# Kernel tuning notes

Hardware: AMD Instinct MI355X
Metric: run time of the kernel (lower is better)

The kernel has to match this reference:

```python
import jax, jax.numpy as jnp
import numpy as np
import math

BS, SEQ, DIM, H, LK = 4, 4096, 768, 12, 256
HD = DIM // H  # 64
WIN = SEQ // LK  # 16, AdaptiveAvgPool1d reduces to uniform windows since SEQ % LK == 0


def setup_inputs() -> dict:
    key = jax.random.key(0)
    ks = jax.random.split(key, 12)
    s = 1.0 / math.sqrt(DIM)
    return {
        "query": jax.random.normal(ks[0], (BS, SEQ, DIM), jnp.float32),
        "key": jax.random.normal(ks[1], (BS, SEQ, DIM), jnp.float32),
        "value": jax.random.normal(ks[2], (BS, SEQ, DIM), jnp.float32),
        "mask": jax.random.normal(ks[3], (BS, SEQ), jnp.float32),  # mask<0 -> padded
        "Wq": jax.random.normal(ks[4], (DIM, DIM), jnp.float32) * s,
        "bq": jnp.zeros((DIM,), jnp.float32),
        "Wk": jax.random.normal(ks[5], (DIM, DIM), jnp.float32) * s,
        "bk": jnp.zeros((DIM,), jnp.float32),
        "Wv": jax.random.normal(ks[6], (DIM, DIM), jnp.float32) * s,
        "bv": jnp.zeros((DIM,), jnp.float32),
        "Wo": jax.random.normal(ks[7], (DIM, DIM), jnp.float32) * s,
        "bo": jnp.zeros((DIM,), jnp.float32),
    }


def reference(query, key, value, mask, Wq, bq, Wk, bk, Wv, bv, Wo, bo):
    bs, q_len, _ = query.shape
    # projections (nn.Linear: x @ W.T + b)
    Q = query @ Wq.T + bq
    K = key @ Wk.T + bk
    V = value @ Wv.T + bv
    # mask-fill padded K/V rows with 0 (mask dim==2 path: bool_mask = mask < 0)
    keep = (mask >= 0)[:, :, None]  # [bs, seq, 1]
    K = jnp.where(keep, K, 0.0)
    V = jnp.where(keep, V, 0.0)
    # adaptive avg pool over sequence -> linformer_k=256 (uniform windows of 16)
    Kc = K.reshape(bs, LK, WIN, DIM).mean(axis=2)  # [bs, 256, dim]
    Vc = V.reshape(bs, LK, WIN, DIM).mean(axis=2)
    # split heads
    Qh = Q.reshape(bs, q_len, H, HD) / math.sqrt(HD)  # scale fused
    Kh = Kc.reshape(bs, LK, H, HD)
    Vh = Vc.reshape(bs, LK, H, HD)
    # low-rank attention: [bs, h, q_len, 256]
    scores = jnp.einsum("bqhd,bkhd->bhqk", Qh, Kh)
    weights = jax.nn.softmax(scores, axis=-1)
    context = jnp.einsum("bhqk,bkhd->bqhd", weights, Vh).reshape(bs, q_len, DIM)
    return context @ Wo.T + bo
```

## Files before the change

kernel.cpp:

```cpp
#include <hip/hip_runtime.h>

#define BS_   4
#define SEQ_  4096
#define DIM_  768
#define NH_   12
#define HD_   64
#define LK_   256

typedef __attribute__((ext_vector_type(8))) short          bf8;
typedef __attribute__((ext_vector_type(8))) unsigned short us8;
typedef __attribute__((ext_vector_type(4))) unsigned short us4;
typedef __attribute__((ext_vector_type(4))) float          f32x4;
typedef __attribute__((ext_vector_type(4))) unsigned int   u32x4;

typedef unsigned int u32g __attribute__((address_space(1)));
typedef unsigned int u32l __attribute__((address_space(3)));

#define LOG2E 1.44269504088896340736f

__device__ __forceinline__ unsigned short f2bf(float f) {
  unsigned u = __builtin_bit_cast(unsigned, f);
  u += 0x7fffu + ((u >> 16) & 1u);
  return (unsigned short)(u >> 16);
}

__device__ __forceinline__ us8 cvt8(const float* __restrict__ p) {
  const float4 a = *(const float4*)p;
  const float4 b = *(const float4*)(p + 4);
  us8 r;
  r[0] = f2bf(a.x); r[1] = f2bf(a.y); r[2] = f2bf(a.z); r[3] = f2bf(a.w);
  r[4] = f2bf(b.x); r[5] = f2bf(b.y); r[6] = f2bf(b.z); r[7] = f2bf(b.w);
  return r;
}

__device__ __forceinline__ f32x4 max4(f32x4 a, f32x4 b) {
  f32x4 r;
  r[0] = fmaxf(a[0], b[0]); r[1] = fmaxf(a[1], b[1]);
  r[2] = fmaxf(a[2], b[2]); r[3] = fmaxf(a[3], b[3]);
  return r;
}

__device__ __forceinline__ float fexp2(float x) {
  float r; asm("v_exp_f32 %0, %1" : "=v"(r) : "v"(x)); return r;
}
__device__ __forceinline__ unsigned cvtpk(float lo, float hi) {
  unsigned r; asm("v_cvt_pk_bf16_f32 %0, %1, %2" : "=v"(r) : "v"(lo), "v"(hi));
  return r;
}

__global__ __launch_bounds__(384) void prep_kernel(
    const float* __restrict__ key, const float* __restrict__ value,
    const float* __restrict__ mask, const float* __restrict__ query,
    const float* __restrict__ Wq, const float* __restrict__ Wk,
    const float* __restrict__ Wv, const float* __restrict__ Wo,
    unsigned short* __restrict__ pk, unsigned short* __restrict__ pv,
    float* __restrict__ frac,
    unsigned short* __restrict__ Qbf, unsigned short* __restrict__ Wbf)
{
  const int bid = blockIdx.x;
  const int tid = threadIdx.x;
  if (bid < 1024) {
    const int b = bid >> 8;
    const int l = bid & 255;
    __shared__ float keep[16];
    if (tid < 16) keep[tid] = (mask[b * SEQ_ + l * 16 + tid] >= 0.f) ? 1.f : 0.f;
    __syncthreads();
    const int isV = tid >= 192;
    const int c = isV ? tid - 192 : tid;
    const float* src = isV ? value : key;
    const float* base = src + (size_t)(b * SEQ_ + l * 16) * DIM_ + c * 4;
    float4 acc = make_float4(0.f, 0.f, 0.f, 0.f);
    #pragma unroll
    for (int w = 0; w < 16; ++w) {
      const float4 v = *(const float4*)(base + (size_t)w * DIM_);
      const float kw = keep[w];
      acc.x = fmaf(kw, v.x, acc.x); acc.y = fmaf(kw, v.y, acc.y);
      acc.z = fmaf(kw, v.z, acc.z); acc.w = fmaf(kw, v.w, acc.w);
    }
    const float s = 1.f / 16.f;
    unsigned short* dst = isV ? pv : pk;
    us4 o4;
    o4[0] = f2bf(acc.x * s); o4[1] = f2bf(acc.y * s);
    o4[2] = f2bf(acc.z * s); o4[3] = f2bf(acc.w * s);
    *(us4*)(dst + (size_t)(b * LK_ + l) * DIM_ + c * 4) = o4;
    if (tid == 0) {
      float cnt = 0.f;
      for (int w = 0; w < 16; ++w) cnt += keep[w];
      frac[b * LK_ + l] = cnt * s;
    }
    return;
  }
  const int QN8 = (BS_ * SEQ_ * DIM_) / 8;
  const int WN8 = (DIM_ * DIM_) / 8;
  const int i0 = (bid - 1024) * 768 + tid;
  #pragma unroll
  for (int u = 0; u < 2; ++u) {
    const int i = i0 + u * 384;
    if (i < QN8) { *(us8*)(Qbf + (size_t)i * 8) = cvt8(query + (size_t)i * 8); continue; }
    int j = i - QN8;
    const float* src; unsigned short* dst;
    if      (j <     WN8) { src = Wq; dst = Wbf;                   }
    else if (j < 2 * WN8) { src = Wk; dst = Wbf + DIM_*DIM_;     j -=     WN8; }
    else if (j < 3 * WN8) { src = Wv; dst = Wbf + 2*DIM_*DIM_;   j -= 2 * WN8; }
    else if (j < 4 * WN8) { src = Wo; dst = Wbf + 3*DIM_*DIM_;   j -= 3 * WN8; }
    else continue;
    *(us8*)(dst + (size_t)j * 8) = cvt8(src + (size_t)j * 8);
  }
}

template<int MODE, int SWZ>
__global__ __launch_bounds__(256) void gemm_bt(
    const void* __restrict__ Aptr_, const void* __restrict__ Bptr_,
    const float* __restrict__ bias, const float* __restrict__ bias2,
    const float* __restrict__ frac,
    void* __restrict__ Cout, float scale)
{
  constexpr int K  = DIM_;
  constexpr int BK = 64;
  constexpr int NT = K / BK;
  __shared__ __align__(16) unsigned short lA[2][128 * BK];
  __shared__ __align__(16) unsigned short lB[2][128 * BK];
  const int tid  = threadIdx.x;
  const int lane = tid & 63;
  const int wave = tid >> 6;

  int bx, by;
  if (SWZ) {
    const int r = (blockIdx.x & 7) * 96 + (blockIdx.x >> 3);
    bx = r / 6; by = r % 6;
  } else {
    bx = blockIdx.x; by = blockIdx.y;
  }
  const int brow = bx * 128;
  const int bcol = by * 128;

  const unsigned short* A  = (const unsigned short*)Aptr_;
  const unsigned short* Bw = (const unsigned short*)Bptr_;
  const float* bb = bias;
  int isV = 0;
  if (MODE == 34) {
    isV = blockIdx.z;
    A  += (size_t)isV * (BS_ * LK_ * DIM_);
    Bw += (size_t)isV * (DIM_ * DIM_);
    if (isV) bb = bias2;
  }

  const int wr = (wave >> 1) * 64;
  const int wc = (wave & 1) * 64;
  const int fr = lane & 15;
  const int hi = lane >> 4;
  const int rx = fr & 7;

  f32x4 acc[4][4];
  #pragma unroll
  for (int i = 0; i < 4; ++i)
    #pragma unroll
    for (int j = 0; j < 4; ++j) acc[i][j] = (f32x4){0.f, 0.f, 0.f, 0.f};

  const int srow = tid >> 3;
  const int schk = ((tid & 7) ^ (srow & 7)) * 8;

  auto STAGE = [&](int t, int b) {
    const int k0 = t * BK;
    #pragma unroll
    for (int s = 0; s < 4; ++s) {
      __builtin_amdgcn_global_load_lds(
          (const u32g*)(A + (size_t)(brow + srow + s * 32) * K + k0 + schk),
          (u32l*)&lA[b][s * 2048 + tid * 8], 16, 0, 0);
      __builtin_amdgcn_global_load_lds(
          (const u32g*)(Bw + (size_t)(bcol + srow + s * 32) * K + k0 + schk),
          (u32l*)&lB[b][s * 2048 + tid * 8], 16, 0, 0);
    }
  };

  auto COMPUTE = [&](int b) {
    #pragma unroll
    for (int ks = 0; ks < 2; ++ks) {
      bf8 af[4], bfv[4];
      const int c = ks * 4 + hi;
      const int pc = (c ^ rx) * 8;
      #pragma unroll
      for (int mi = 0; mi < 4; ++mi)
        af[mi] = *(const bf8*)&lA[b][(wr + mi * 16 + fr) * BK + pc];
      #pragma unroll
      for (int ni = 0; ni < 4; ++ni)
        bfv[ni] = *(const bf8*)&lB[b][(wc + ni * 16 + fr) * BK + pc];
      #pragma unroll
      for (int mi = 0; mi < 4; ++mi)
        #pragma unroll
        for (int ni = 0; ni < 4; ++ni)
          acc[mi][ni] = __builtin_amdgcn_mfma_f32_16x16x32_bf16(af[mi], bfv[ni], acc[mi][ni], 0, 0, 0);
    }
  };

  STAGE(0, 0);
  STAGE(1, 1);
  asm volatile("s_waitcnt vmcnt(8)" ::: "memory");
  __builtin_amdgcn_s_barrier();

  #pragma unroll 2
  for (int t = 0; t < NT; ++t) {
    COMPUTE(t & 1);
    if (t + 1 < NT) {
      __builtin_amdgcn_s_barrier();
      if (t + 2 < NT) {
        STAGE(t + 2, t & 1);
        asm volatile("s_waitcnt vmcnt(8)" ::: "memory");
      } else {
        asm volatile("s_waitcnt vmcnt(0)" ::: "memory");
      }
      __builtin_amdgcn_s_barrier();
    }
  }

  const int er = (lane >> 4) * 4;
  #pragma unroll
  for (int mi = 0; mi < 4; ++mi) {
    #pragma unroll
    for (int ni = 0; ni < 4; ++ni) {
      #pragma unroll
      for (int j = 0; j < 4; ++j) {
        const int r = brow + wr + mi * 16 + er + j;
        const int c = bcol + wc + ni * 16 + fr;
        float v = acc[mi][ni][j];
        if (MODE == 0) {
          v = (v + bias[c]) * scale;
          ((unsigned short*)Cout)[(size_t)r * DIM_ + c] = f2bf(v);
        } else if (MODE == 2) {
          ((float*)Cout)[(size_t)r * DIM_ + c] = v + bias[c];
        } else {
          v += frac[r] * bb[c];
          const int bb_ = r >> 8, key = r & 255;
          const int hh = c >> 6, dd = c & 63;
          const int bh = bb_ * NH_ + hh;
          size_t idx;
          if (isV) {
            idx = (size_t)bh * 16384 +
                ((key >> 5) * 4 + (dd >> 4)) * 512 + ((key >> 3) & 3) * 128 +
                (dd & 15) * 8 + (key & 7) + 786432;
          } else {
            const int tt = key >> 5, g = (key >> 3) & 3, sub = (key >> 2) & 1, jj = key & 3;
            const int frk = g * 4 + jj;
            idx = (size_t)bh * 16384 +
                (((tt * 2 + sub) * 2) + (dd >> 5)) * 512 + ((dd >> 3) & 3) * 128 +
                frk * 8 + (dd & 7);
          }
          ((unsigned short*)Cout)[idx] = f2bf(v);
        }
      }
    }
  }
}

__global__ __launch_bounds__(512, 4) void attn_fused(
    const unsigned short* __restrict__ Qh,
    const unsigned short* __restrict__ Kf,
    const unsigned short* __restrict__ Vf,
    unsigned short* __restrict__ ctx)
{
  __shared__ __align__(16) unsigned short Ks[16384];
  const int tid  = threadIdx.x;
  const int lane = tid & 63;
  const int wave = tid >> 6;
  const int bh = blockIdx.y;
  const int b = bh / NH_, h = bh % NH_;
  const int fr = lane & 15;
  const int hi = lane >> 4;
  const int qrow = blockIdx.x * 128 + wave * 16;

  {
    const unsigned short* kg = Kf + (size_t)bh * 16384 + tid * 8;
    #pragma unroll
    for (int i = 0; i < 4; ++i)
      __builtin_amdgcn_global_load_lds((const u32g*)(kg + i * 4096),
                                       (u32l*)&Ks[i * 4096 + tid * 8], 16, 0, 0);
  }

  const unsigned short* qp = Qh + (size_t)(b * SEQ_ + qrow + fr) * DIM_ + h * HD_ + hi * 8;
  const bf8 q0 = *(const bf8*)qp;
  const bf8 q1 = *(const bf8*)(qp + 32);

  __syncthreads();

  f32x4 scA[8], scB[8];
  __builtin_amdgcn_s_setprio(1);
  #pragma unroll
  for (int s = 0; s < 8; ++s) {
    const bf8 ka0 = *(const bf8*)&Ks[(s * 4 + 0) * 512 + lane * 8];
    const bf8 ka1 = *(const bf8*)&Ks[(s * 4 + 1) * 512 + lane * 8];
    const bf8 kb0 = *(const bf8*)&Ks[(s * 4 + 2) * 512 + lane * 8];
    const bf8 kb1 = *(const bf8*)&Ks[(s * 4 + 3) * 512 + lane * 8];
    f32x4 x = (f32x4){0.f, 0.f, 0.f, 0.f};
    x = __builtin_amdgcn_mfma_f32_16x16x32_bf16(ka0, q0, x, 0, 0, 0);
    x = __builtin_amdgcn_mfma_f32_16x16x32_bf16(ka1, q1, x, 0, 0, 0);
    scA[s] = x;
    f32x4 y = (f32x4){0.f, 0.f, 0.f, 0.f};
    y = __builtin_amdgcn_mfma_f32_16x16x32_bf16(kb0, q0, y, 0, 0, 0);
    y = __builtin_amdgcn_mfma_f32_16x16x32_bf16(kb1, q1, y, 0, 0, 0);
    scB[s] = y;
  }
  __builtin_amdgcn_s_setprio(0);

  f32x4 tm[8];
  #pragma unroll
  for (int s = 0; s < 8; ++s) tm[s] = max4(scA[s], scB[s]);
  tm[0] = max4(tm[0], tm[4]); tm[1] = max4(tm[1], tm[5]);
  tm[2] = max4(tm[2], tm[6]); tm[3] = max4(tm[3], tm[7]);
  tm[0] = max4(tm[0], tm[2]); tm[1] = max4(tm[1], tm[3]);
  tm[0] = max4(tm[0], tm[1]);
  float m = fmaxf(fmaxf(tm[0][0], tm[0][1]), fmaxf(tm[0][2], tm[0][3]));
  m = fmaxf(m, __shfl_xor(m, 16));
  m = fmaxf(m, __shfl_xor(m, 32));

  f32x4 uA = (f32x4){0.f, 0.f, 0.f, 0.f};
  f32x4 uB = (f32x4){0.f, 0.f, 0.f, 0.f};
  #pragma unroll
  for (int s = 0; s < 8; ++s) {
    #pragma unroll
    for (int j = 0; j < 4; ++j) {
      scA[s][j] = fexp2(scA[s][j] - m);
      scB[s][j] = fexp2(scB[s][j] - m);
    }
    uA += scA[s];
    uB += scB[s];
  }
  const f32x4 uv = uA + uB;
  float sum = (uv[0] + uv[1]) + (uv[2] + uv[3]);
  sum += __shfl_xor(sum, 16);
  sum += __shfl_xor(sum, 32);
  const float inv = 1.f / sum;

  bf8 pa[8];
  #pragma unroll
  for (int s = 0; s < 8; ++s) {
    u32x4 w;
    w[0] = cvtpk(scA[s][0] * inv, scA[s][1] * inv);
    w[1] = cvtpk(scA[s][2] * inv, scA[s][3] * inv);
    w[2] = cvtpk(scB[s][0] * inv, scB[s][1] * inv);
    w[3] = cvtpk(scB[s][2] * inv, scB[s][3] * inv);
    pa[s] = __builtin_bit_cast(bf8, w);
  }

  const unsigned short* vb = Vf + (size_t)bh * 16384 + lane * 8;
  f32x4 acc[4];
  #pragma unroll
  for (int ct = 0; ct < 4; ++ct) acc[ct] = (f32x4){0.f, 0.f, 0.f, 0.f};
  __builtin_amdgcn_s_setprio(1);
  #pragma unroll
  for (int s = 0; s < 8; ++s) {
    #pragma unroll
    for (int ct = 0; ct < 4; ++ct) {
      const bf8 vf = *(const bf8*)(vb + (s * 4 + ct) * 512);
      acc[ct] = __builtin_amdgcn_mfma_f32_16x16x32_bf16(pa[s], vf, acc[ct], 0, 0, 0);
    }
  }
  __builtin_amdgcn_s_setprio(0);

  #pragma unroll
  for (int ct = 0; ct < 4; ++ct)
    #pragma unroll
    for (int j = 0; j < 4; ++j)
      ctx[(size_t)(b * SEQ_ + qrow + hi * 4 + j) * DIM_ + h * HD_ + ct * 16 + fr] =
          f2bf(acc[ct][j]);
}

extern "C" void kernel_launch(void* const* d_in, const int* in_sizes, int n_in,
                              void* d_out, int out_size, void* d_ws, size_t ws_size,
                              hipStream_t stream) {
  const float* query = (const float*)d_in[0];
  const float* key   = (const float*)d_in[1];
  const float* value = (const float*)d_in[2];
  const float* mask  = (const float*)d_in[3];
  const float* Wq    = (const float*)d_in[4];
  const float* bq    = (const float*)d_in[5];
  const float* Wk    = (const float*)d_in[6];
  const float* bk    = (const float*)d_in[7];
  const float* Wv    = (const float*)d_in[8];
  const float* bv    = (const float*)d_in[9];
  const float* Wo    = (const float*)d_in[10];
  const float* bo    = (const float*)d_in[11];
  float* out = (float*)d_out;

  char* ws = (char*)d_ws;
  unsigned short* Qh  = (unsigned short*)ws;
  unsigned short* ctx = (unsigned short*)(ws + 25165824);
  unsigned short* pK  = (unsigned short*)(ws + 50331648);
  unsigned short* pV  = (unsigned short*)(ws + 51904512);
  unsigned short* Kf  = (unsigned short*)(ws + 53477376);
  unsigned short* Vf  = (unsigned short*)(ws + 55050240);
  float*          frac = (float*)(ws + 56623104);
  unsigned short* Wbf = (unsigned short*)(ws + 56627200);
  unsigned short* Qbf = ctx;

  const float qscale = 0.125f * LOG2E;

  prep_kernel<<<dim3(3456), dim3(384), 0, stream>>>(
      key, value, mask, query, Wq, Wk, Wv, Wo, pK, pV, frac, Qbf, Wbf);
  gemm_bt<0, 1><<<dim3(768), dim3(256), 0, stream>>>(
      Qbf, Wbf, bq, nullptr, nullptr, Qh, qscale);
  gemm_bt<34, 0><<<dim3(8, 6, 2), dim3(256), 0, stream>>>(
      pK, Wbf + DIM_*DIM_, bk, bv, frac, Kf, 1.f);
  attn_fused<<<dim3(32, 48), dim3(512), 0, stream>>>(Qh, Kf, Vf, ctx);
  gemm_bt<2, 1><<<dim3(768), dim3(256), 0, stream>>>(
      ctx, Wbf + 3*DIM_*DIM_, bo, nullptr, nullptr, out, 1.f);
}
```

Before: 134.3 us.

## Skip loading masked K/V rows in pooling and double per-block work in prep

The pooling part of the prep kernel now builds a compacted list of unmasked rows per window and loads only those rows, padded to a multiple of 8, so padded K/V rows are never fetched from memory. Each block now handles two pooled windows, and the conversion blocks each process four chunks instead of two, which halves the grid size. Since about half the mask values are negative, this aims to cut K/V read traffic roughly in half. In exchange it adds shared-memory setup, a serial list-building step and data-dependent indexed loads.

```diff
diff --git a/kernel.cpp b/kernel.cpp
--- a/kernel.cpp
+++ b/kernel.cpp
@@ -59,42 +59,65 @@
 {
   const int bid = blockIdx.x;
   const int tid = threadIdx.x;
-  if (bid < 1024) {
-    const int b = bid >> 8;
-    const int l = bid & 255;
-    __shared__ float keep[16];
-    if (tid < 16) keep[tid] = (mask[b * SEQ_ + l * 16 + tid] >= 0.f) ? 1.f : 0.f;
+  if (bid < 512) {
+    const int g0 = bid * 2;
+    const int b  = g0 >> 8;
+    const int l0 = g0 & 255;
+    __shared__ float keep[2][16];
+    __shared__ int   wlist[2][16];
+    __shared__ float wwt[2][16];
+    __shared__ int   nk[2];
+    if (tid < 32)
+      keep[tid >> 4][tid & 15] =
+          (mask[b * SEQ_ + (l0 + (tid >> 4)) * 16 + (tid & 15)] >= 0.f) ? 1.f : 0.f;
     __syncthreads();
+    if (tid < 2) {
+      const int w = tid;
+      int n = 0; float cnt = 0.f;
+      for (int i = 0; i < 16; ++i)
+        if (keep[w][i] != 0.f) { wlist[w][n] = i; wwt[w][n] = 1.f; ++n; cnt += 1.f; }
+      frac[b * LK_ + l0 + w] = cnt * (1.f / 16.f);
+      const int pad = (n == 0) ? 0 : wlist[w][0];
+      for (int i = n; i < 16; ++i) { wlist[w][i] = pad; wwt[w][i] = 0.f; }
+      nk[w] = (n == 0) ? 0 : ((n + 7) & ~7);
+    }
+    __syncthreads();
+    const int nkmax = nk[0] > nk[1] ? nk[0] : nk[1];
     const int isV = tid >= 192;
     const int c = isV ? tid - 192 : tid;
     const float* src = isV ? value : key;
-    const float* base = src + (size_t)(b * SEQ_ + l * 16) * DIM_ + c * 4;
-    float4 acc = make_float4(0.f, 0.f, 0.f, 0.f);
-    #pragma unroll
-    for (int w = 0; w < 16; ++w) {
-      const float4 v = *(const float4*)(base + (size_t)w * DIM_);
-      const float kw = keep[w];
-      acc.x = fmaf(kw, v.x, acc.x); acc.y = fmaf(kw, v.y, acc.y);
-      acc.z = fmaf(kw, v.z, acc.z); acc.w = fmaf(kw, v.w, acc.w);
+    const float* base0 = src + (size_t)(b * SEQ_ + l0 * 16) * DIM_ + c * 4;
+    const float* base1 = base0 + (size_t)16 * DIM_;
+    float4 a0 = make_float4(0.f, 0.f, 0.f, 0.f);
+    float4 a1 = make_float4(0.f, 0.f, 0.f, 0.f);
+    for (int i = 0; i < nkmax; i += 8) {
+      #pragma unroll
+      for (int u = 0; u < 8; ++u) {
+        const float4 v0 = *(const float4*)(base0 + (size_t)wlist[0][i + u] * DIM_);
+        const float4 v1 = *(const float4*)(base1 + (size_t)wlist[1][i + u] * DIM_);
+        const float w0 = wwt[0][i + u], w1 = wwt[1][i + u];
+        a0.x = fmaf(w0, v0.x, a0.x); a0.y = fmaf(w0, v0.y, a0.y);
+        a0.z = fmaf(w0, v0.z, a0.z); a0.w = fmaf(w0, v0.w, a0.w);
+        a1.x = fmaf(w1, v1.x, a1.x); a1.y = fmaf(w1, v1.y, a1.y);
+        a1.z = fmaf(w1, v1.z, a1.z); a1.w = fmaf(w1, v1.w, a1.w);
+      }
     }
     const float s = 1.f / 16.f;
     unsigned short* dst = isV ? pv : pk;
-    us4 o4;
-    o4[0] = f2bf(acc.x * s); o4[1] = f2bf(acc.y * s);
-    o4[2] = f2bf(acc.z * s); o4[3] = f2bf(acc.w * s);
-    *(us4*)(dst + (size_t)(b * LK_ + l) * DIM_ + c * 4) = o4;
-    if (tid == 0) {
-      float cnt = 0.f;
-      for (int w = 0; w < 16; ++w) cnt += keep[w];
-      frac[b * LK_ + l] = cnt * s;
-    }
+    us4 o0, o1;
+    o0[0] = f2bf(a0.x * s); o0[1] = f2bf(a0.y * s);
+    o0[2] = f2bf(a0.z * s); o0[3] = f2bf(a0.w * s);
+    o1[0] = f2bf(a1.x * s); o1[1] = f2bf(a1.y * s);
+    o1[2] = f2bf(a1.z * s); o1[3] = f2bf(a1.w * s);
+    *(us4*)(dst + (size_t)(b * LK_ + l0)     * DIM_ + c * 4) = o0;
+    *(us4*)(dst + (size_t)(b * LK_ + l0 + 1) * DIM_ + c * 4) = o1;
     return;
   }
   const int QN8 = (BS_ * SEQ_ * DIM_) / 8;
   const int WN8 = (DIM_ * DIM_) / 8;
-  const int i0 = (bid - 1024) * 768 + tid;
-  #pragma unroll
-  for (int u = 0; u < 2; ++u) {
+  const int i0 = (bid - 512) * 1536 + tid;
+  #pragma unroll
+  for (int u = 0; u < 4; ++u) {
     const int i = i0 + u * 384;
     if (i < QN8) { *(us8*)(Qbf + (size_t)i * 8) = cvt8(query + (size_t)i * 8); continue; }
     int j = i - QN8;
@@ -394,7 +417,7 @@
 
   const float qscale = 0.125f * LOG2E;
 
-  prep_kernel<<<dim3(3456), dim3(384), 0, stream>>>(
+  prep_kernel<<<dim3(1728), dim3(384), 0, stream>>>(
       key, value, mask, query, Wq, Wk, Wv, Wo, pK, pV, frac, Qbf, Wbf);
   gemm_bt<0, 1><<<dim3(768), dim3(256), 0, stream>>>(
       Qbf, Wbf, bq, nullptr, nullptr, Qh, qscale);
```

Result: faster. 127.8 us (-4.8%).
